# Kernel tuning notes

Measured on AMD Instinct MI355X. Metric: run time of the kernel, lower is better.

Reference implementation:

```python
import math
import jax, jax.numpy as jnp
import numpy as np

HIDDEN = 1024
N_HEADS = 16
HEAD = HIDDEN // N_HEADS
B = 2
L = 2048
STRIDE = 128
EXPR = 8
MAXPOS = 2048


def _checkpoint(wi):
    if wi % STRIDE == 0 and wi != 0:
        return wi - EXPR
    return (wi // STRIDE) * STRIDE + STRIDE - EXPR


def _subset_summaries(absolute_max):
    ci = _checkpoint(0)
    s = set()
    while ci <= absolute_max - 1:
        s |= set(range(ci, min(ci + EXPR + 1, absolute_max)))
        ci = _checkpoint(ci + STRIDE)
    return s


def build_sparse_mask(n, bidirectional=True):
    # Faithful numpy port of prepare_sparse_mask: -1e4 everywhere, 0 at allowed positions.
    mask = np.full((n, n), -10000.0, dtype=np.float32)
    global_summaries = _subset_summaries(n) if bidirectional else set()
    for i in range(n):
        absolute_max = n if bidirectional else i + 1
        rounded = ((i + STRIDE) // STRIDE) * STRIDE
        if i % STRIDE == 0 and i != 0:
            s1 = set(range(i - STRIDE, min(absolute_max, i + 1)))
        else:
            s1 = set(range(max(0, rounded - STRIDE), min(absolute_max, rounded + 1)))
        s2 = set() if bidirectional else _subset_summaries(absolute_max)
        idx = sorted(s1 | s2 | global_summaries)
        mask[i, idx] = 0.0
    return mask


def setup_inputs() -> dict:
    key = jax.random.key(0)
    ks = jax.random.split(key, 8)
    s = 1.0 / math.sqrt(HIDDEN)
    inp = {
        "hidden_states": jax.random.normal(ks[0], (B, L, HIDDEN), dtype=jnp.float32),
        "attention_mask": jnp.zeros((B, 1, 1, L), dtype=jnp.float32),
        "Wq": jax.random.normal(ks[1], (HIDDEN, HIDDEN), dtype=jnp.float32) * s,
        "bq": jnp.zeros((HIDDEN,), dtype=jnp.float32),
        "Wk": jax.random.normal(ks[2], (HIDDEN, HIDDEN), dtype=jnp.float32) * s,
        "bk": jnp.zeros((HIDDEN,), dtype=jnp.float32),
        "Wv": jax.random.normal(ks[3], (HIDDEN, HIDDEN), dtype=jnp.float32) * s,
        "bv": jnp.zeros((HIDDEN,), dtype=jnp.float32),
        "sparse_mask": jnp.asarray(build_sparse_mask(MAXPOS)[:L, :L]),
    }
    return inp


def _split_heads(x):  # [B, L, H] -> [B, nH, L, hd]
    b, l, _ = x.shape
    return x.reshape(b, l, N_HEADS, HEAD).transpose(0, 2, 1, 3)


def reference(hidden_states, attention_mask, Wq, bq, Wk, bk, Wv, bv, sparse_mask):
    q = _split_heads(hidden_states @ Wq + bq)
    k = _split_heads(hidden_states @ Wk + bk)
    v = _split_heads(hidden_states @ Wv + bv)
    scores = jnp.einsum("bhqd,bhkd->bhqk", q, k) / math.sqrt(HEAD)
    scores = scores + sparse_mask  # [L,L] broadcasts over [B,nH,L,L]
    scores = jnp.clip(scores, -10000.0, 10000.0)
    scores = scores + attention_mask
    probs = jax.nn.softmax(scores.astype(jnp.float32), axis=-1).astype(scores.dtype)
    # dropout prob = 0.0 -> identity
    ctx = jnp.einsum("bhqk,bhkd->bhqd", probs, v)
    return ctx.transpose(0, 2, 1, 3).reshape(hidden_states.shape[0], -1, HIDDEN)
```

## Files before the change

### kernel.cpp

```cpp
#include <hip/hip_runtime.h>

#define HID 1024
#define NH 16
#define HD 64
#define BB 2
#define LL 2048
#define GC 143
#define GP 192
#define AMT_PER_B 2240

typedef __attribute__((ext_vector_type(8))) __bf16 bf16x8;
typedef __attribute__((ext_vector_type(4))) float f32x4;
typedef __attribute__((ext_vector_type(4))) int i32x4;

__device__ __forceinline__ void gload_lds16(const void* g, void* l) {
  __builtin_amdgcn_global_load_lds((const __attribute__((address_space(1))) void*)g,
                                   (__attribute__((address_space(3))) void*)l, 16, 0, 0);
}

__device__ __forceinline__ unsigned int cvtpk(float lo, float hi) {
  unsigned int r;
  asm("v_cvt_pk_bf16_f32 %0, %1, %2" : "=v"(r) : "v"(lo), "v"(hi));
  return r;
}

__global__ __launch_bounds__(256) void prep_kernel(
    const float* __restrict__ hs, __bf16* __restrict__ hsb,
    const float* __restrict__ Wq, const float* __restrict__ Wk,
    const float* __restrict__ Wv, __bf16* __restrict__ wtb,
    const float* __restrict__ amask, unsigned int* __restrict__ zbase,
    float* __restrict__ amt) {
  int bx = blockIdx.x;
  int t = threadIdx.x;
  if (bx < 2048) {
    int i = bx * 256 + t;
    const float4* src = (const float4*)hs;
    float4 a = src[2 * i], b = src[2 * i + 1];
    bf16x8 v;
    v[0] = (__bf16)a.x; v[1] = (__bf16)a.y; v[2] = (__bf16)a.z; v[3] = (__bf16)a.w;
    v[4] = (__bf16)b.x; v[5] = (__bf16)b.y; v[6] = (__bf16)b.z; v[7] = (__bf16)b.w;
    ((bf16x8*)hsb)[i] = v;
  } else if (bx < 2048 + 768) {
    int z3 = bx - 2048;
    int kt = z3 & 15, nt = (z3 >> 4) & 15, z = z3 >> 8;
    const float* w = (z == 0) ? Wq : (z == 1) ? Wk : Wv;
    __bf16* dst = wtb + (size_t)z * HID * HID;
    __shared__ __bf16 tile[64][66];
    int cr = t & 63, rr = t >> 6;
#pragma unroll
    for (int it = 0; it < 16; it++) {
      int r = it * 4 + rr;
      tile[cr][r] = (__bf16)w[(size_t)(kt * 64 + r) * HID + nt * 64 + cr];
    }
    __syncthreads();
#pragma unroll
    for (int it = 0; it < 16; it++) {
      int r = it * 4 + rr;
      dst[(size_t)(nt * 64 + r) * HID + kt * 64 + cr] = tile[r][cr];
    }
  } else if (bx < 2048 + 768 + 1536) {
    int i = (bx - 2816) * 256 + t;
    zbase[i] = 0u;
  } else {
    int idx = (bx - 4352) * 256 + t;
    if (idx < BB * AMT_PER_B) {
      int b = idx / AMT_PER_B, r = idx % AMT_PER_B;
      float val;
      if (r < GP) {
        int k = r / 9, j = r - 9 * k;
        val = (r < GC) ? (amask[b * LL + 120 + 128 * k + j] - 20.f) : -1e5f;
      } else {
        int r2 = r - GP;
        int w = r2 >> 7, off = r2 & 127;
        bool gcol = (off >= 120) || (off == 0 && w != 0);
        val = gcol ? -1e5f : (amask[b * LL + w * 128 + off] - 20.f);
      }
      amt[idx] = val;
    }
  }
}

__global__ __launch_bounds__(256, 2) void qkv_gemm_kernel(
    const __bf16* __restrict__ hsb, const __bf16* __restrict__ wtb,
    const float* __restrict__ bq, const float* __restrict__ bk,
    const float* __restrict__ bv, __bf16* __restrict__ qb,
    __bf16* __restrict__ kkb, __bf16* __restrict__ vtb,
    __bf16* __restrict__ kgb, __bf16* __restrict__ vgb) {
  int nt = blockIdx.x, mt = blockIdx.y, which = blockIdx.z;
  const __bf16* wt = wtb + (size_t)which * HID * HID;
  const float* bias = (which == 0) ? bq : (which == 1) ? bk : bv;

  __shared__ __bf16 a_lds[128 * 64];
  __shared__ __bf16 b_lds[128 * 64];

  int tid = threadIdx.x;
  int wave = tid >> 6, lane = tid & 63;
  int wm = wave >> 1, wn = wave & 1;
  int lrow = lane & 15, lgr = lane >> 4, g = lane & 7;

  f32x4 acc[4][4];
#pragma unroll
  for (int i = 0; i < 4; i++)
#pragma unroll
    for (int j = 0; j < 4; j++) acc[i][j] = f32x4{0.f, 0.f, 0.f, 0.f};

  for (int kk = 0; kk < HID; kk += 64) {
#pragma unroll
    for (int i = 0; i < 4; i++) {
      int r = (wave * 4 + i) * 8 + (lane >> 3);
      int gs = (g ^ (r & 7)) * 8;
      gload_lds16(hsb + (size_t)(mt * 128 + r) * HID + kk + gs,
                  &a_lds[(wave * 4 + i) * 512]);
      gload_lds16(wt + (size_t)(nt * 128 + r) * HID + kk + gs,
                  &b_lds[(wave * 4 + i) * 512]);
    }
    __syncthreads();
#pragma unroll
    for (int kf = 0; kf < 2; kf++) {
      bf16x8 af[4], bfr[4];
#pragma unroll
      for (int mr = 0; mr < 4; mr++) {
        int row = wm * 64 + mr * 16 + lrow;
        af[mr] = *(const bf16x8*)((const char*)a_lds + row * 128 +
                                  ((kf * 64 + lgr * 16) ^ ((row & 7) << 4)));
      }
#pragma unroll
      for (int nr = 0; nr < 4; nr++) {
        int row = wn * 64 + nr * 16 + lrow;
        bfr[nr] = *(const bf16x8*)((const char*)b_lds + row * 128 +
                                   ((kf * 64 + lgr * 16) ^ ((row & 7) << 4)));
      }
#pragma unroll
      for (int mr = 0; mr < 4; mr++)
#pragma unroll
        for (int nr = 0; nr < 4; nr++)
          acc[mr][nr] = __builtin_amdgcn_mfma_f32_16x16x32_bf16(
              af[mr], bfr[nr], acc[mr][nr], 0, 0, 0);
    }
    __syncthreads();
  }

#pragma unroll
  for (int nr = 0; nr < 4; nr++) {
    int n = nt * 128 + wn * 64 + nr * 16 + lrow;
    float bsv = bias[n];
    int hh = n >> 6, d = n & 63;
#pragma unroll
    for (int mr = 0; mr < 4; mr++) {
#pragma unroll
      for (int reg = 0; reg < 4; reg++) {
        int m = mt * 128 + wm * 64 + mr * 16 + lgr * 4 + reg;
        int bidx = m >> 11, l = m & 2047;
        float val = acc[mr][nr][reg] + bsv;
        int c7 = l & 127;
        bool isg = (c7 >= 120) || (c7 == 0 && l != 0);
        int cidx = (c7 >= 120) ? ((l >> 7) * 9 + (c7 - 120)) : (((l >> 7) - 1) * 9 + 8);
        if (which == 0) {
          val *= 0.125f;
          qb[((size_t)(bidx * NH + hh) * LL + l) * HD + d] = (__bf16)val;
        } else if (which == 1) {
          __bf16 bv16 = (__bf16)val;
          kkb[((size_t)(bidx * NH + hh) * LL + l) * HD + d] = bv16;
          if (isg) kgb[((size_t)(bidx * NH + hh) * GP + cidx) * HD + d] = bv16;
        } else {
          __bf16 bv16 = (__bf16)val;
          vtb[((size_t)(bidx * NH + hh) * HD + d) * LL + l] = bv16;
          if (isg) vgb[((size_t)(bidx * NH + hh) * HD + d) * GP + cidx] = bv16;
        }
      }
    }
  }
}

__global__ __launch_bounds__(256, 4) void attn_kernel(
    const __bf16* __restrict__ qb, const __bf16* __restrict__ kkb,
    const __bf16* __restrict__ vtb, const __bf16* __restrict__ kgb,
    const __bf16* __restrict__ vgb, const float* __restrict__ amt,
    float* __restrict__ out) {
  __shared__ __bf16 kbuf[2][64 * 64];
  __shared__ __bf16 vbuf[2][64 * 64];

  int qt = blockIdx.x, hh = blockIdx.y, b = blockIdx.z;
  int tid = threadIdx.x, wave = tid >> 6, lane = tid & 63;
  int lrow = lane & 15, lgr = lane >> 4, g = lane & 7;

  const __bf16* qbh = qb + (size_t)(b * NH + hh) * LL * HD;
  const __bf16* kbh = kkb + (size_t)(b * NH + hh) * LL * HD;
  const __bf16* vth = vtb + (size_t)(b * NH + hh) * HD * LL;
  const __bf16* kgh = kgb + (size_t)(b * NH + hh) * GP * HD;
  const __bf16* vgh = vgb + (size_t)(b * NH + hh) * HD * GP;

  int shift = (qt == 16) ? 0 : 1;
  int qt2 = (qt == 16) ? 0 : qt;
  int W = qt2 * 128;
  const float* amt_b = amt + b * AMT_PER_B;
  const float* amt_l = amt_b + GP + qt2 * 128;

  int qrowA = qt2 * 128 + shift + wave * 32 + lrow;
  int qrowB = qrowA + 16;
  int qldA = (qrowA > LL - 1) ? (LL - 1) : qrowA;
  int qldB = (qrowB > LL - 1) ? (LL - 1) : qrowB;
  bf16x8 qA0 = *(const bf16x8*)(qbh + (size_t)qldA * HD + lgr * 8);
  bf16x8 qA1 = *(const bf16x8*)(qbh + (size_t)qldA * HD + 32 + lgr * 8);
  bf16x8 qB0 = *(const bf16x8*)(qbh + (size_t)qldB * HD + lgr * 8);
  bf16x8 qB1 = *(const bf16x8*)(qbh + (size_t)qldB * HD + 32 + lgr * 8);

  int va = ((lgr & 1) * 32 + lrow) * 4;
  int vb = va + 64;
  bool lohalf = (lane < 32);

  float lA = 0.f, lB = 0.f;
  f32x4 oA[4], oB[4];
#pragma unroll
  for (int i = 0; i < 4; i++) {
    oA[i] = f32x4{0.f, 0.f, 0.f, 0.f};
    oB[i] = f32x4{0.f, 0.f, 0.f, 0.f};
  }

#define STAGE(IT, BI)                                                     \
  do {                                                                    \
    const __bf16 *ks_, *vs_;                                              \
    int vst_;                                                             \
    if ((IT) < 3) {                                                       \
      ks_ = kgh + (size_t)((IT)*64) * HD;                                 \
      vs_ = vgh + (IT)*64;                                                \
      vst_ = GP;                                                          \
    } else {                                                              \
      int cb_ = W + ((IT)-3) * 64;                                        \
      ks_ = kbh + (size_t)cb_ * HD;                                       \
      vs_ = vth + cb_;                                                    \
      vst_ = LL;                                                          \
    }                                                                     \
    _Pragma("unroll")                                                     \
    for (int i_ = 0; i_ < 2; i_++) {                                      \
      int r_ = (wave * 2 + i_) * 8 + (lane >> 3);                         \
      int gs_ = (g ^ (r_ & 7)) * 8;                                       \
      gload_lds16(ks_ + (size_t)r_ * HD + gs_, &kbuf[BI][(wave * 2 + i_) * 512]); \
      gload_lds16(vs_ + (size_t)r_ * vst_ + gs_, &vbuf[BI][(wave * 2 + i_) * 512]); \
    }                                                                     \
  } while (0)

  STAGE(0, 0);
  __syncthreads();

#pragma unroll
  for (int it = 0; it < 5; it++) {
    int cur = it & 1;
    if (it < 4) STAGE(it + 1, cur ^ 1);

    const __bf16* k_lds = kbuf[cur];
    const __bf16* v_lds = vbuf[cur];

    const float* abase = (it < 3) ? (amt_b + it * 64) : (amt_l + (it - 3) * 64);
    f32x4 ad[4];
#pragma unroll
    for (int nr = 0; nr < 4; nr++)
      ad[nr] = *(const f32x4*)(abase + nr * 16 + lgr * 4);

    f32x4 sA[4], sB[4];
#pragma unroll
    for (int nr = 0; nr < 4; nr++) {
      int row = nr * 16 + lrow;
      bf16x8 kf0 = *(const bf16x8*)((const char*)k_lds + row * 128 +
                                    ((lgr * 16) ^ ((row & 7) << 4)));
      bf16x8 kf1 = *(const bf16x8*)((const char*)k_lds + row * 128 +
                                    ((64 + lgr * 16) ^ ((row & 7) << 4)));
      f32x4 zA = f32x4{0.f, 0.f, 0.f, 0.f};
      zA = __builtin_amdgcn_mfma_f32_16x16x32_bf16(kf0, qA0, zA, 0, 0, 0);
      zA = __builtin_amdgcn_mfma_f32_16x16x32_bf16(kf1, qA1, zA, 0, 0, 0);
      sA[nr] = zA;
      f32x4 zB = f32x4{0.f, 0.f, 0.f, 0.f};
      zB = __builtin_amdgcn_mfma_f32_16x16x32_bf16(kf0, qB0, zB, 0, 0, 0);
      zB = __builtin_amdgcn_mfma_f32_16x16x32_bf16(kf1, qB1, zB, 0, 0, 0);
      sB[nr] = zB;
    }

#pragma unroll
    for (int nr = 0; nr < 4; nr++) {
#pragma unroll
      for (int reg = 0; reg < 4; reg++) {
        float vA = fminf(fmaxf(sA[nr][reg], -10000.f), 10000.f) + ad[nr][reg];
        float pA = __expf(vA);
        sA[nr][reg] = pA;
        lA += pA;
        float vB = fminf(fmaxf(sB[nr][reg], -10000.f), 10000.f) + ad[nr][reg];
        float pB = __expf(vB);
        sB[nr][reg] = pB;
        lB += pB;
      }
    }

    bf16x8 pbA0, pbA1, pbB0, pbB1;
    {
      unsigned int c00 = cvtpk(sA[0][0], sA[0][1]), c01 = cvtpk(sA[0][2], sA[0][3]);
      unsigned int c10 = cvtpk(sA[1][0], sA[1][1]), c11 = cvtpk(sA[1][2], sA[1][3]);
      unsigned int c20 = cvtpk(sA[2][0], sA[2][1]), c21 = cvtpk(sA[2][2], sA[2][3]);
      unsigned int c30 = cvtpk(sA[3][0], sA[3][1]), c31 = cvtpk(sA[3][2], sA[3][3]);
      i32x4 w0, w1;
      int a0 = __builtin_amdgcn_ds_bpermute(va, (int)c00);
      int a1 = __builtin_amdgcn_ds_bpermute(va, (int)c10);
      w0[0] = lohalf ? a0 : a1;
      int b0 = __builtin_amdgcn_ds_bpermute(va, (int)c01);
      int b1 = __builtin_amdgcn_ds_bpermute(va, (int)c11);
      w0[1] = lohalf ? b0 : b1;
      int d0 = __builtin_amdgcn_ds_bpermute(vb, (int)c00);
      int d1 = __builtin_amdgcn_ds_bpermute(vb, (int)c10);
      w0[2] = lohalf ? d0 : d1;
      int e0 = __builtin_amdgcn_ds_bpermute(vb, (int)c01);
      int e1 = __builtin_amdgcn_ds_bpermute(vb, (int)c11);
      w0[3] = lohalf ? e0 : e1;
      int f0 = __builtin_amdgcn_ds_bpermute(va, (int)c20);
      int f1 = __builtin_amdgcn_ds_bpermute(va, (int)c30);
      w1[0] = lohalf ? f0 : f1;
      int g0 = __builtin_amdgcn_ds_bpermute(va, (int)c21);
      int g1 = __builtin_amdgcn_ds_bpermute(va, (int)c31);
      w1[1] = lohalf ? g0 : g1;
      int h0 = __builtin_amdgcn_ds_bpermute(vb, (int)c20);
      int h1 = __builtin_amdgcn_ds_bpermute(vb, (int)c30);
      w1[2] = lohalf ? h0 : h1;
      int i0 = __builtin_amdgcn_ds_bpermute(vb, (int)c21);
      int i1 = __builtin_amdgcn_ds_bpermute(vb, (int)c31);
      w1[3] = lohalf ? i0 : i1;
      pbA0 = __builtin_bit_cast(bf16x8, w0);
      pbA1 = __builtin_bit_cast(bf16x8, w1);
    }
    {
      unsigned int c00 = cvtpk(sB[0][0], sB[0][1]), c01 = cvtpk(sB[0][2], sB[0][3]);
      unsigned int c10 = cvtpk(sB[1][0], sB[1][1]), c11 = cvtpk(sB[1][2], sB[1][3]);
      unsigned int c20 = cvtpk(sB[2][0], sB[2][1]), c21 = cvtpk(sB[2][2], sB[2][3]);
      unsigned int c30 = cvtpk(sB[3][0], sB[3][1]), c31 = cvtpk(sB[3][2], sB[3][3]);
      i32x4 w0, w1;
      int a0 = __builtin_amdgcn_ds_bpermute(va, (int)c00);
      int a1 = __builtin_amdgcn_ds_bpermute(va, (int)c10);
      w0[0] = lohalf ? a0 : a1;
      int b0 = __builtin_amdgcn_ds_bpermute(va, (int)c01);
      int b1 = __builtin_amdgcn_ds_bpermute(va, (int)c11);
      w0[1] = lohalf ? b0 : b1;
      int d0 = __builtin_amdgcn_ds_bpermute(vb, (int)c00);
      int d1 = __builtin_amdgcn_ds_bpermute(vb, (int)c10);
      w0[2] = lohalf ? d0 : d1;
      int e0 = __builtin_amdgcn_ds_bpermute(vb, (int)c01);
      int e1 = __builtin_amdgcn_ds_bpermute(vb, (int)c11);
      w0[3] = lohalf ? e0 : e1;
      int f0 = __builtin_amdgcn_ds_bpermute(va, (int)c20);
      int f1 = __builtin_amdgcn_ds_bpermute(va, (int)c30);
      w1[0] = lohalf ? f0 : f1;
      int g0 = __builtin_amdgcn_ds_bpermute(va, (int)c21);
      int g1 = __builtin_amdgcn_ds_bpermute(va, (int)c31);
      w1[1] = lohalf ? g0 : g1;
      int h0 = __builtin_amdgcn_ds_bpermute(vb, (int)c20);
      int h1 = __builtin_amdgcn_ds_bpermute(vb, (int)c30);
      w1[2] = lohalf ? h0 : h1;
      int i0 = __builtin_amdgcn_ds_bpermute(vb, (int)c21);
      int i1 = __builtin_amdgcn_ds_bpermute(vb, (int)c31);
      w1[3] = lohalf ? i0 : i1;
      pbB0 = __builtin_bit_cast(bf16x8, w0);
      pbB1 = __builtin_bit_cast(bf16x8, w1);
    }

#pragma unroll
    for (int nd = 0; nd < 4; nd++) {
      int row = nd * 16 + lrow;
      bf16x8 vf0 = *(const bf16x8*)((const char*)v_lds + row * 128 +
                                    ((lgr * 16) ^ ((row & 7) << 4)));
      bf16x8 vf1 = *(const bf16x8*)((const char*)v_lds + row * 128 +
                                    ((64 + lgr * 16) ^ ((row & 7) << 4)));
      oA[nd] = __builtin_amdgcn_mfma_f32_16x16x32_bf16(vf0, pbA0, oA[nd], 0, 0, 0);
      oA[nd] = __builtin_amdgcn_mfma_f32_16x16x32_bf16(vf1, pbA1, oA[nd], 0, 0, 0);
      oB[nd] = __builtin_amdgcn_mfma_f32_16x16x32_bf16(vf0, pbB0, oB[nd], 0, 0, 0);
      oB[nd] = __builtin_amdgcn_mfma_f32_16x16x32_bf16(vf1, pbB1, oB[nd], 0, 0, 0);
    }
    if (it < 4) __syncthreads();
  }
#undef STAGE

  lA += __shfl_xor(lA, 16);
  lA += __shfl_xor(lA, 32);
  lB += __shfl_xor(lB, 16);
  lB += __shfl_xor(lB, 32);
  float rlA = 1.f / lA, rlB = 1.f / lB;

  if (qrowA < LL) {
    float* obase = out + ((size_t)b * LL + qrowA) * HID + hh * HD + lgr * 4;
#pragma unroll
    for (int nd = 0; nd < 4; nd++) {
      float4 ov;
      ov.x = oA[nd][0] * rlA;
      ov.y = oA[nd][1] * rlA;
      ov.z = oA[nd][2] * rlA;
      ov.w = oA[nd][3] * rlA;
      *(float4*)(obase + nd * 16) = ov;
    }
  }
  if (qrowB < LL) {
    float* obase = out + ((size_t)b * LL + qrowB) * HID + hh * HD + lgr * 4;
#pragma unroll
    for (int nd = 0; nd < 4; nd++) {
      float4 ov;
      ov.x = oB[nd][0] * rlB;
      ov.y = oB[nd][1] * rlB;
      ov.z = oB[nd][2] * rlB;
      ov.w = oB[nd][3] * rlB;
      *(float4*)(obase + nd * 16) = ov;
    }
  }
}

extern "C" void kernel_launch(void* const* d_in, const int* in_sizes, int n_in,
                              void* d_out, int out_size, void* d_ws, size_t ws_size,
                              hipStream_t stream) {
  (void)in_sizes; (void)n_in; (void)out_size; (void)ws_size;
  const float* hs = (const float*)d_in[0];
  const float* amask = (const float*)d_in[1];
  const float* Wq = (const float*)d_in[2];
  const float* bq = (const float*)d_in[3];
  const float* Wk = (const float*)d_in[4];
  const float* bk = (const float*)d_in[5];
  const float* Wv = (const float*)d_in[6];
  const float* bv = (const float*)d_in[7];
  float* out = (float*)d_out;

  char* ws = (char*)d_ws;
  __bf16* hsb = (__bf16*)(ws);
  __bf16* wtb = (__bf16*)(ws + 8388608);
  __bf16* qb  = (__bf16*)(ws + 14680064);
  __bf16* kb  = (__bf16*)(ws + 23068672);
  __bf16* vtb = (__bf16*)(ws + 31457280);
  __bf16* kgb = (__bf16*)(ws + 39845888);
  __bf16* vgb = (__bf16*)(ws + 40632320);
  float*  amt = (float*)(ws + 41418752);

  hipLaunchKernelGGL(prep_kernel, dim3(4370), dim3(256), 0, stream,
                     hs, hsb, Wq, Wk, Wv, wtb, amask, (unsigned int*)kgb, amt);
  hipLaunchKernelGGL(qkv_gemm_kernel, dim3(8, 32, 3), dim3(256), 0, stream,
                     hsb, wtb, bq, bk, bv, qb, kb, vtb, kgb, vgb);
  hipLaunchKernelGGL(attn_kernel, dim3(17, NH, BB), dim3(256), 0, stream,
                     qb, kb, vtb, kgb, vgb, amt, out);
}
```

Measured before the change: 70.27 us.

## Replace P-fragment bpermute shuffles with permuted V fragment loads and set MFMA priority

Removes the 32 ds_bpermute cross-lane shuffles per iteration that rearranged the bf16 probability fragments into the MFMA B-operand layout. Instead P is packed directly from the score accumulator layout, and V is read from LDS as two 8-byte pieces per fragment so that its k-index ordering matches P's native layout. It also raises wave priority around the MFMA blocks with s_setprio. The cost is twice as many, narrower LDS reads for V, which may raise bank conflicts.

Result: no change. 69.45 us (median of 2 runs) (-1.2%).

```diff
diff --git a/kernel.cpp b/kernel.cpp
--- a/kernel.cpp
+++ b/kernel.cpp
@@ -12,6 +12,7 @@
 typedef __attribute__((ext_vector_type(8))) __bf16 bf16x8;
 typedef __attribute__((ext_vector_type(4))) float f32x4;
 typedef __attribute__((ext_vector_type(4))) int i32x4;
+typedef __attribute__((ext_vector_type(2))) unsigned long long u64x2;
 
 __device__ __forceinline__ void gload_lds16(const void* g, void* l) {
   __builtin_amdgcn_global_load_lds((const __attribute__((address_space(1))) void*)g,
@@ -22,6 +23,18 @@
   unsigned int r;
   asm("v_cvt_pk_bf16_f32 %0, %1, %2" : "=v"(r) : "v"(lo), "v"(hi));
   return r;
+}
+
+__device__ __forceinline__ bf16x8 vfrag(const char* vbase, int r, int gA, int gB,
+                                        int half) {
+  unsigned long long lo =
+      *(const unsigned long long*)(vbase + r * 128 + ((gA ^ (r & 7)) << 4) + half);
+  unsigned long long hi =
+      *(const unsigned long long*)(vbase + r * 128 + ((gB ^ (r & 7)) << 4) + half);
+  u64x2 u;
+  u[0] = lo;
+  u[1] = hi;
+  return __builtin_bit_cast(bf16x8, u);
 }
 
 __global__ __launch_bounds__(256) void prep_kernel(
@@ -205,9 +218,7 @@
   bf16x8 qB0 = *(const bf16x8*)(qbh + (size_t)qldB * HD + lgr * 8);
   bf16x8 qB1 = *(const bf16x8*)(qbh + (size_t)qldB * HD + 32 + lgr * 8);
 
-  int va = ((lgr & 1) * 32 + lrow) * 4;
-  int vb = va + 64;
-  bool lohalf = (lane < 32);
+  int g0 = lgr >> 1, half = (lgr & 1) * 8;
 
   float lA = 0.f, lB = 0.f;
   f32x4 oA[4], oB[4];
@@ -249,7 +260,7 @@
     if (it < 4) STAGE(it + 1, cur ^ 1);
 
     const __bf16* k_lds = kbuf[cur];
-    const __bf16* v_lds = vbuf[cur];
+    const char* v_ldsc = (const char*)vbuf[cur];
 
     const float* abase = (it < 3) ? (amt_b + it * 64) : (amt_l + (it - 3) * 64);
     f32x4 ad[4];
@@ -258,6 +269,7 @@
       ad[nr] = *(const f32x4*)(abase + nr * 16 + lgr * 4);
 
     f32x4 sA[4], sB[4];
+    __builtin_amdgcn_s_setprio(1);
 #pragma unroll
     for (int nr = 0; nr < 4; nr++) {
       int row = nr * 16 + lrow;
@@ -274,6 +286,7 @@
       zB = __builtin_amdgcn_mfma_f32_16x16x32_bf16(kf1, qB1, zB, 0, 0, 0);
       sB[nr] = zB;
     }
+    __builtin_amdgcn_s_setprio(0);
 
 #pragma unroll
     for (int nr = 0; nr < 4; nr++) {
@@ -290,86 +303,40 @@
       }
     }
 
-    bf16x8 pbA0, pbA1, pbB0, pbB1;
-    {
-      unsigned int c00 = cvtpk(sA[0][0], sA[0][1]), c01 = cvtpk(sA[0][2], sA[0][3]);
-      unsigned int c10 = cvtpk(sA[1][0], sA[1][1]), c11 = cvtpk(sA[1][2], sA[1][3]);
-      unsigned int c20 = cvtpk(sA[2][0], sA[2][1]), c21 = cvtpk(sA[2][2], sA[2][3]);
-      unsigned int c30 = cvtpk(sA[3][0], sA[3][1]), c31 = cvtpk(sA[3][2], sA[3][3]);
-      i32x4 w0, w1;
-      int a0 = __builtin_amdgcn_ds_bpermute(va, (int)c00);
-      int a1 = __builtin_amdgcn_ds_bpermute(va, (int)c10);
-      w0[0] = lohalf ? a0 : a1;
-      int b0 = __builtin_amdgcn_ds_bpermute(va, (int)c01);
-      int b1 = __builtin_amdgcn_ds_bpermute(va, (int)c11);
-      w0[1] = lohalf ? b0 : b1;
-      int d0 = __builtin_amdgcn_ds_bpermute(vb, (int)c00);
-      int d1 = __builtin_amdgcn_ds_bpermute(vb, (int)c10);
-      w0[2] = lohalf ? d0 : d1;
-      int e0 = __builtin_amdgcn_ds_bpermute(vb, (int)c01);
-      int e1 = __builtin_amdgcn_ds_bpermute(vb, (int)c11);
-      w0[3] = lohalf ? e0 : e1;
-      int f0 = __builtin_amdgcn_ds_bpermute(va, (int)c20);
-      int f1 = __builtin_amdgcn_ds_bpermute(va, (int)c30);
-      w1[0] = lohalf ? f0 : f1;
-      int g0 = __builtin_amdgcn_ds_bpermute(va, (int)c21);
-      int g1 = __builtin_amdgcn_ds_bpermute(va, (int)c31);
-      w1[1] = lohalf ? g0 : g1;
-      int h0 = __builtin_amdgcn_ds_bpermute(vb, (int)c20);
-      int h1 = __builtin_amdgcn_ds_bpermute(vb, (int)c30);
-      w1[2] = lohalf ? h0 : h1;
-      int i0 = __builtin_amdgcn_ds_bpermute(vb, (int)c21);
-      int i1 = __builtin_amdgcn_ds_bpermute(vb, (int)c31);
-      w1[3] = lohalf ? i0 : i1;
-      pbA0 = __builtin_bit_cast(bf16x8, w0);
-      pbA1 = __builtin_bit_cast(bf16x8, w1);
-    }
-    {
-      unsigned int c00 = cvtpk(sB[0][0], sB[0][1]), c01 = cvtpk(sB[0][2], sB[0][3]);
-      unsigned int c10 = cvtpk(sB[1][0], sB[1][1]), c11 = cvtpk(sB[1][2], sB[1][3]);
-      unsigned int c20 = cvtpk(sB[2][0], sB[2][1]), c21 = cvtpk(sB[2][2], sB[2][3]);
-      unsigned int c30 = cvtpk(sB[3][0], sB[3][1]), c31 = cvtpk(sB[3][2], sB[3][3]);
-      i32x4 w0, w1;
-      int a0 = __builtin_amdgcn_ds_bpermute(va, (int)c00);
-      int a1 = __builtin_amdgcn_ds_bpermute(va, (int)c10);
-      w0[0] = lohalf ? a0 : a1;
-      int b0 = __builtin_amdgcn_ds_bpermute(va, (int)c01);
-      int b1 = __builtin_amdgcn_ds_bpermute(va, (int)c11);
-      w0[1] = lohalf ? b0 : b1;
-      int d0 = __builtin_amdgcn_ds_bpermute(vb, (int)c00);
-      int d1 = __builtin_amdgcn_ds_bpermute(vb, (int)c10);
-      w0[2] = lohalf ? d0 : d1;
-      int e0 = __builtin_amdgcn_ds_bpermute(vb, (int)c01);
-      int e1 = __builtin_amdgcn_ds_bpermute(vb, (int)c11);
-      w0[3] = lohalf ? e0 : e1;
-      int f0 = __builtin_amdgcn_ds_bpermute(va, (int)c20);
-      int f1 = __builtin_amdgcn_ds_bpermute(va, (int)c30);
-      w1[0] = lohalf ? f0 : f1;
-      int g0 = __builtin_amdgcn_ds_bpermute(va, (int)c21);
-      int g1 = __builtin_amdgcn_ds_bpermute(va, (int)c31);
-      w1[1] = lohalf ? g0 : g1;
-      int h0 = __builtin_amdgcn_ds_bpermute(vb, (int)c20);
-      int h1 = __builtin_amdgcn_ds_bpermute(vb, (int)c30);
-      w1[2] = lohalf ? h0 : h1;
-      int i0 = __builtin_amdgcn_ds_bpermute(vb, (int)c21);
-      int i1 = __builtin_amdgcn_ds_bpermute(vb, (int)c31);
-      w1[3] = lohalf ? i0 : i1;
-      pbB0 = __builtin_bit_cast(bf16x8, w0);
-      pbB1 = __builtin_bit_cast(bf16x8, w1);
-    }
-
+    i32x4 wA0, wA1, wB0, wB1;
+    wA0[0] = (int)cvtpk(sA[0][0], sA[0][1]);
+    wA0[1] = (int)cvtpk(sA[0][2], sA[0][3]);
+    wA0[2] = (int)cvtpk(sA[1][0], sA[1][1]);
+    wA0[3] = (int)cvtpk(sA[1][2], sA[1][3]);
+    wA1[0] = (int)cvtpk(sA[2][0], sA[2][1]);
+    wA1[1] = (int)cvtpk(sA[2][2], sA[2][3]);
+    wA1[2] = (int)cvtpk(sA[3][0], sA[3][1]);
+    wA1[3] = (int)cvtpk(sA[3][2], sA[3][3]);
+    wB0[0] = (int)cvtpk(sB[0][0], sB[0][1]);
+    wB0[1] = (int)cvtpk(sB[0][2], sB[0][3]);
+    wB0[2] = (int)cvtpk(sB[1][0], sB[1][1]);
+    wB0[3] = (int)cvtpk(sB[1][2], sB[1][3]);
+    wB1[0] = (int)cvtpk(sB[2][0], sB[2][1]);
+    wB1[1] = (int)cvtpk(sB[2][2], sB[2][3]);
+    wB1[2] = (int)cvtpk(sB[3][0], sB[3][1]);
+    wB1[3] = (int)cvtpk(sB[3][2], sB[3][3]);
+    bf16x8 pbA0 = __builtin_bit_cast(bf16x8, wA0);
+    bf16x8 pbA1 = __builtin_bit_cast(bf16x8, wA1);
+    bf16x8 pbB0 = __builtin_bit_cast(bf16x8, wB0);
+    bf16x8 pbB1 = __builtin_bit_cast(bf16x8, wB1);
+
+    __builtin_amdgcn_s_setprio(1);
 #pragma unroll
     for (int nd = 0; nd < 4; nd++) {
       int row = nd * 16 + lrow;
-      bf16x8 vf0 = *(const bf16x8*)((const char*)v_lds + row * 128 +
-                                    ((lgr * 16) ^ ((row & 7) << 4)));
-      bf16x8 vf1 = *(const bf16x8*)((const char*)v_lds + row * 128 +
-                                    ((64 + lgr * 16) ^ ((row & 7) << 4)));
-      oA[nd] = __builtin_amdgcn_mfma_f32_16x16x32_bf16(vf0, pbA0, oA[nd], 0, 0, 0);
-      oA[nd] = __builtin_amdgcn_mfma_f32_16x16x32_bf16(vf1, pbA1, oA[nd], 0, 0, 0);
-      oB[nd] = __builtin_amdgcn_mfma_f32_16x16x32_bf16(vf0, pbB0, oB[nd], 0, 0, 0);
-      oB[nd] = __builtin_amdgcn_mfma_f32_16x16x32_bf16(vf1, pbB1, oB[nd], 0, 0, 0);
-    }
+      bf16x8 va0 = vfrag(v_ldsc, row, g0, 2 + g0, half);
+      bf16x8 va1 = vfrag(v_ldsc, row, 4 + g0, 6 + g0, half);
+      oA[nd] = __builtin_amdgcn_mfma_f32_16x16x32_bf16(va0, pbA0, oA[nd], 0, 0, 0);
+      oA[nd] = __builtin_amdgcn_mfma_f32_16x16x32_bf16(va1, pbA1, oA[nd], 0, 0, 0);
+      oB[nd] = __builtin_amdgcn_mfma_f32_16x16x32_bf16(va0, pbB0, oB[nd], 0, 0, 0);
+      oB[nd] = __builtin_amdgcn_mfma_f32_16x16x32_bf16(va1, pbB1, oB[nd], 0, 0, 0);
+    }
+    __builtin_amdgcn_s_setprio(0);
     if (it < 4) __syncthreads();
   }
 #undef STAGE
```
